# Kernel optimization log

Hardware: AMD Instinct MI355X
Metric: run time of the kernel (lower is better)

## Reference

```python
import jax, jax.numpy as jnp
import numpy as np

B, T, D, H_, N_ = 4, 1024, 2048, 32, 64


def setup_inputs() -> dict:
    key = jax.random.key(0)
    keys = iter(jax.random.split(key, 40))

    def rn(shape, s):
        return (jax.random.normal(next(keys), shape, jnp.float32) * s)

    inp = {
        'x': rn((B, T, D), 1.0),
        'x_prev': jnp.zeros((B, D), jnp.float32),
        'v_first': rn((B, T, D), 1.0),
        'state': jnp.zeros((B, H_, N_, N_), jnp.float32),
        'x_r': rn((1, 1, D), 0.1), 'x_w': rn((1, 1, D), 0.1), 'x_k': rn((1, 1, D), 0.1),
        'x_v': rn((1, 1, D), 0.1), 'x_a': rn((1, 1, D), 0.1), 'x_g': rn((1, 1, D), 0.1),
        'w0': rn((1, 1, D), 0.5),
        'w1': rn((D, 64), 0.02), 'w2': rn((64, D), 0.02),
        'a0': rn((1, 1, D), 0.5),
        'a1': rn((D, 64), 0.02), 'a2': rn((64, D), 0.02),
        'v0': rn((1, 1, D), 0.5),
        'v1': rn((D, 32), 0.02), 'v2': rn((32, D), 0.02),
        'g1': rn((D, 128), 0.02), 'g2': rn((128, D), 0.02),
        'k_k': rn((1, 1, D), 0.5), 'k_a': rn((1, 1, D), 0.5),
        'r_k': rn((D,), 0.5),
        'R_': rn((D, D), 0.02), 'K_': rn((D, D), 0.02),
        'V_': rn((D, D), 0.02), 'O_': rn((D, D), 0.02),
        'ln_w': jnp.ones((D,), jnp.float32),
        'ln_b': jnp.zeros((D,), jnp.float32),
        'H': H_, 'N': N_, 'layer_id': 1,
    }
    return inp


def reference(x, x_prev, v_first, state, x_r, x_w, x_k, x_v, x_a, x_g,
              w0, w1, w2, a0, a1, a2, v0, v1, v2, g1, g2,
              k_k, k_a, r_k, R_, K_, V_, O_, ln_w, ln_b, H, N, layer_id):
    B, T, D = x.shape
    # token shift
    xx = jnp.concatenate([x_prev[:, None, :], x[:, :-1]], axis=1) - x
    xr = x + xx * x_r; xw = x + xx * x_w; xk = x + xx * x_k
    xv = x + xx * x_v; xa = x + xx * x_a; xg = x + xx * x_g

    r = xr @ R_
    # decay: exp(-e^{-0.5} * sigmoid(.)) == exp(-exp(logsigmoid(.) - 0.5))
    w = jnp.exp(-0.606531 * jax.nn.sigmoid(w0 + jnp.tanh(xw @ w1) @ w2))
    k = xk @ K_
    v = xv @ V_
    a = jax.nn.sigmoid(a0 + (xa @ a1) @ a2)
    g = jax.nn.sigmoid(xg @ g1) @ g2

    kk4 = (k * k_k).reshape(B, T, H, N)
    kk4 = kk4 / jnp.maximum(jnp.linalg.norm(kk4, axis=-1, keepdims=True), 1e-12)
    kk = kk4.reshape(B, T, D)
    k = k * (1 + (a - 1) * k_a)
    if layer_id == 0:
        v_first = v
    else:
        v = v + (v_first - v) * jax.nn.sigmoid(v0 + (xv @ v1) @ v2)

    aa = -kk
    bb = kk * a

    def to_tbhn(t):
        return t.reshape(B, T, H, N).transpose(1, 0, 2, 3)

    rs, ws, ks, vs, aas, bbs = map(to_tbhn, (r, w, k, v, aa, bb))

    def step(st, inp):
        r_t, w_t, k_t, v_t, a_t, b_t = inp
        ab = jnp.einsum('bhi,bhj->bhij', a_t, b_t)      # rank-1 removal/add
        vk = jnp.einsum('bhi,bhj->bhij', v_t, k_t)
        st = st * w_t[:, :, None, :] + jnp.einsum('bhik,bhkj->bhij', st, ab) + vk
        y = jnp.einsum('bhij,bhj->bhi', st, r_t)        # state @ r
        return st, y

    state_f, ys = jax.lax.scan(step, state, (rs, ws, ks, vs, aas, bbs))
    y = ys.transpose(1, 0, 2, 3)  # [B,T,H,N]

    # torch group_norm on [B, H*N, T]: normalize each (b,h) group over (N,T)
    mean = y.mean(axis=(1, 3), keepdims=True)
    var = y.var(axis=(1, 3), keepdims=True)
    y = (y - mean) / jnp.sqrt(var + 0.00064)
    y = y * ln_w.reshape(1, 1, H, N) + ln_b.reshape(1, 1, H, N)

    bonus = (r * k * r_k).reshape(B, T, H, N).sum(-1, keepdims=True) * v.reshape(B, T, H, N)
    xx_fin = (y + bonus).reshape(B, T, D)
    out = (xx_fin * g) @ O_
    return out, x[:, -1], state_f, v_first
```

## Files before the change

kernel.cpp:

```cpp
#include <hip/hip_runtime.h>
#include <math.h>
#include <stdint.h>

#define B_ 4
#define T_ 1024
#define D_ 2048
#define H_ 32
#define N_ 64
static constexpr size_t BTD = (size_t)B_ * T_ * D_;

typedef __attribute__((ext_vector_type(8))) short short8;
typedef __attribute__((ext_vector_type(4))) float floatx4;

typedef __attribute__((address_space(3))) unsigned int       lds_u32;
typedef __attribute__((address_space(1))) const unsigned int glb_u32;

__device__ __forceinline__ void async_cp16(const unsigned short* g, unsigned short* l) {
  __builtin_amdgcn_global_load_lds((glb_u32*)g, (lds_u32*)l, 16, 0, 0);
}

__device__ __forceinline__ unsigned short f2bf(float f) {
  union { float f; unsigned int u; } v; v.f = f;
  unsigned int r = v.u + 0x7fffu + ((v.u >> 16) & 1u);
  return (unsigned short)(r >> 16);
}

__device__ __forceinline__ float bf2f(unsigned short u) {
  union { unsigned int u; float f; } v; v.u = (unsigned int)u << 16;
  return v.f;
}

__device__ __forceinline__ void store_bf4(unsigned short* dst, float a, float b, float c, float d) {
  unsigned long long v = (unsigned long long)f2bf(a) | ((unsigned long long)f2bf(b) << 16)
                       | ((unsigned long long)f2bf(c) << 32) | ((unsigned long long)f2bf(d) << 48);
  *(unsigned long long*)dst = v;
}

__device__ __forceinline__ void ld_bf8(const unsigned short* p, float* o) {
  union { short8 v; unsigned short u[8]; } t;
  t.v = *(const short8*)p;
#pragma unroll
  for (int c = 0; c < 8; ++c) o[c] = bf2f(t.u[c]);
}

__device__ __forceinline__ void cv4(uint2 r, float* o) {
  union { unsigned int u; float f; } t;
  t.u = r.x << 16;         o[0] = t.f;
  t.u = r.x & 0xffff0000u; o[1] = t.f;
  t.u = r.y << 16;         o[2] = t.f;
  t.u = r.y & 0xffff0000u; o[3] = t.f;
}

__device__ __forceinline__ float sigm(float z) { return 1.f / (1.f + expf(-z)); }

__global__ __launch_bounds__(256)
void mix_kernel(const float* __restrict__ x, const float* __restrict__ xprev,
                const float* __restrict__ coef, unsigned short* __restrict__ out)
{
  size_t i4 = (size_t)blockIdx.x * 256 + threadIdx.x;
  size_t e = i4 * 4;
  if (e >= BTD) return;
  int d = (int)(e & (D_ - 1));
  size_t bt = e >> 11;
  int t = (int)(bt & (T_ - 1));
  float4 xv = *(const float4*)(x + e);
  float4 xs;
  if (t == 0) xs = *(const float4*)(xprev + ((bt >> 10) << 11) + d);
  else        xs = *(const float4*)(x + e - D_);
  float4 cf = *(const float4*)(coef + d);
  float o0 = xv.x + (xs.x - xv.x) * cf.x;
  float o1 = xv.y + (xs.y - xv.y) * cf.y;
  float o2 = xv.z + (xs.z - xv.z) * cf.z;
  float o3 = xv.w + (xs.w - xv.w) * cf.w;
  store_bf4(out + e, o0, o1, o2, o3);
}

__global__ __launch_bounds__(256)
void transpose_bf16(const float* sA, const float* sB, const float* sC, const float* sD,
                    unsigned short* dA, unsigned short* dB, unsigned short* dC, unsigned short* dD,
                    int R, int C, int Cout)
{
  const float* src = blockIdx.z == 0 ? sA : blockIdx.z == 1 ? sB : blockIdx.z == 2 ? sC : sD;
  unsigned short* dst = blockIdx.z == 0 ? dA : blockIdx.z == 1 ? dB : blockIdx.z == 2 ? dC : dD;
  __shared__ float tile[64][65];
  int rBase = blockIdx.x * 64;
  int cBase = blockIdx.y * 64;
  int tid = threadIdx.x;
  int tc = tid & 63, tr4 = tid >> 6;
#pragma unroll
  for (int jj = 0; jj < 16; ++jj) {
    int r = rBase + jj * 4 + tr4;
    int c = cBase + tc;
    float v = (r < R && c < C) ? src[(size_t)r * C + c] : 0.f;
    tile[jj * 4 + tr4][tc] = v;
  }
  __syncthreads();
#pragma unroll
  for (int jj = 0; jj < 16; ++jj) {
    int cl = jj * 4 + tr4;
    int rl = tc;
    int c = cBase + cl, r = rBase + rl;
    if (c < Cout && r < R)
      dst[(size_t)c * R + r] = f2bf(tile[rl][cl]);
  }
}

template<int EPI>
__global__ __launch_bounds__(256, 2)
void gemm_bt(const unsigned short* __restrict__ A, const unsigned short* __restrict__ BT,
             float* __restrict__ Cf, unsigned short* __restrict__ Cb,
             int K, int ldc, int Nout, const float* __restrict__ bias)
{
  __shared__ unsigned short lA[128 * 32];
  __shared__ unsigned short lB[128 * 32];
  int tid = threadIdx.x;
  int lane = tid & 63;
  int wv = tid >> 6;
  int wrow = wv >> 1, wcol = wv & 1;
  int mBase = blockIdx.x * 128;
  int nBase = blockIdx.y * 128;
  int r16 = lane & 15, q = lane >> 4;

  floatx4 acc[4][4];
  floatx4 zero = {0.f, 0.f, 0.f, 0.f};
#pragma unroll
  for (int i = 0; i < 4; i++)
#pragma unroll
    for (int j = 0; j < 4; j++) acc[i][j] = zero;

  int arow = tid >> 2, ach = (tid & 3) * 8;
  const unsigned short* ga0 = A  + (size_t)(mBase + arow) * K + ach;
  const unsigned short* ga1 = A  + (size_t)(mBase + 64 + arow) * K + ach;
  const unsigned short* gb0 = BT + (size_t)(nBase + arow) * K + ach;
  const unsigned short* gb1 = BT + (size_t)(nBase + 64 + arow) * K + ach;
  unsigned short* la0 = lA + tid * 8;
  unsigned short* la1 = lA + 2048 + tid * 8;
  unsigned short* lb0 = lB + tid * 8;
  unsigned short* lb1 = lB + 2048 + tid * 8;

  for (int kb = 0; kb < K; kb += 32) {
    async_cp16(ga0 + kb, la0);
    async_cp16(ga1 + kb, la1);
    async_cp16(gb0 + kb, lb0);
    async_cp16(gb1 + kb, lb1);
    __syncthreads();
    short8 af[4], bf[4];
#pragma unroll
    for (int i = 0; i < 4; i++)
      af[i] = *(const short8*)(lA + (wrow * 64 + i * 16 + r16) * 32 + q * 8);
#pragma unroll
    for (int j = 0; j < 4; j++)
      bf[j] = *(const short8*)(lB + (wcol * 64 + j * 16 + r16) * 32 + q * 8);
#pragma unroll
    for (int i = 0; i < 4; i++)
#pragma unroll
      for (int j = 0; j < 4; j++)
        acc[i][j] = __builtin_amdgcn_mfma_f32_16x16x32_bf16(af[i], bf[j], acc[i][j], 0, 0, 0);
    __syncthreads();
  }

#pragma unroll
  for (int i = 0; i < 4; i++) {
    int r0 = mBase + wrow * 64 + i * 16 + q * 4;
#pragma unroll
    for (int j = 0; j < 4; j++) {
      int c = nBase + wcol * 64 + j * 16 + r16;
#pragma unroll
      for (int rg = 0; rg < 4; rg++) {
        float v = acc[i][j][rg];
        size_t idx = (size_t)(r0 + rg) * ldc + c;
        if (EPI == 0) {
          Cf[idx] = v;
        } else if (EPI == 1) {
          if (c < Nout) Cb[idx] = f2bf(tanhf(v));
        } else if (EPI == 2) {
          if (c < Nout) Cb[idx] = f2bf(sigm(v));
        } else if (EPI == 3) {
          if (c < Nout) Cb[idx] = f2bf(v);
        } else if (EPI == 6) {
          Cb[idx] = f2bf(sigm(bias[c] + v));
        } else if (EPI == 7) {
          Cb[idx] = f2bf(expf(-0.606531f * sigm(bias[c] + v)));
        }
      }
    }
  }
}

__global__ __launch_bounds__(256)
void prep_kernel(unsigned short* __restrict__ kb, unsigned short* __restrict__ ab,
                 float* __restrict__ vb, unsigned short* __restrict__ vmb,
                 const float* __restrict__ vfirst, const float* __restrict__ kkc,
                 const float* __restrict__ kac, const int* __restrict__ layer)
{
  int g = blockIdx.x * 4 + (threadIdx.x >> 6);
  int n = threadIdx.x & 63;
  size_t idx = (size_t)g * 64 + n;
  int d = ((g & (H_ - 1)) << 6) + n;
  float kr = bf2f(kb[idx]);
  float av = bf2f(ab[idx]);
  float vr = vb[idx];
  float vm = bf2f(vmb[idx]);
  float vf = vfirst[idx];
  float kkv = kr * kkc[d];
  float ss = kkv * kkv;
#pragma unroll
  for (int m = 1; m < 64; m <<= 1) ss += __shfl_xor(ss, m);
  float nrm = fmaxf(sqrtf(ss), 1e-12f);
  kkv = kkv / nrm;
  float kf = kr * (1.f + (av - 1.f) * kac[d]);
  float vfin = (*layer == 0) ? vr : vr + (vf - vr) * vm;
  kb[idx] = f2bf(kf);
  vb[idx] = vfin;
  ab[idx] = f2bf(-kkv);
  vmb[idx] = f2bf(kkv * av);
}

__global__ __launch_bounds__(256, 2)
void scan_kernel(const unsigned short* __restrict__ rb, const unsigned short* __restrict__ wb,
                 const unsigned short* __restrict__ kb, const float* __restrict__ vb,
                 const unsigned short* __restrict__ ab, const unsigned short* __restrict__ bbv,
                 const float* __restrict__ s0, float* __restrict__ yb,
                 float* __restrict__ sf)
{
  int blk = blockIdx.x;
  int bh = blk >> 2;
  int quarter = blk & 3;
  int b = bh >> 5, h = bh & 31;
  int tid = threadIdx.x;
  int lane = tid & 63;
  int wvi = tid >> 6;
  int i = quarter * 16 + wvi * 4 + (lane >> 4);
  int p = lane & 15;
  int co = p * 4;

  float st[4];
  {
    const float* sp = s0 + ((size_t)bh * 64 + i) * 64 + co;
    *(float4*)st = *(const float4*)sp;
  }
  size_t base = (size_t)b * T_ * D_ + h * 64;
  const unsigned short* pr = rb + base + co;
  const unsigned short* pw = wb + base + co;
  const unsigned short* pk = kb + base + co;
  const unsigned short* pa = ab + base + co;
  const unsigned short* pb = bbv + base + co;
  const float* pv = vb + base + i;
  float* py = yb + base + i;

  uint2 rgR[8], rgW[8], rgK[8], rgA[8], rgB[8];
  float rgV[8];
#pragma unroll
  for (int s = 0; s < 8; ++s) {
    size_t o = (size_t)s * D_;
    rgR[s] = *(const uint2*)(pr + o);
    rgW[s] = *(const uint2*)(pw + o);
    rgK[s] = *(const uint2*)(pk + o);
    rgA[s] = *(const uint2*)(pa + o);
    rgB[s] = *(const uint2*)(pb + o);
    rgV[s] = pv[o];
  }

  for (int tb = 0; tb < T_; tb += 8) {
#pragma unroll
    for (int s = 0; s < 8; ++s) {
      int t = tb + s;
      size_t o = (size_t)t * D_;
      float av[4], wv4[4], kv[4], bv[4], rv[4];
      cv4(rgA[s], av);
      cv4(rgW[s], wv4);
      cv4(rgK[s], kv);
      cv4(rgB[s], bv);
      cv4(rgR[s], rv);
      float vi = rgV[s];

      int tn = t + 8;
      size_t on = (size_t)(tn < T_ ? tn : 0) * D_;
      rgR[s] = *(const uint2*)(pr + on);
      rgW[s] = *(const uint2*)(pw + on);
      rgK[s] = *(const uint2*)(pk + on);
      rgA[s] = *(const uint2*)(pa + on);
      rgB[s] = *(const uint2*)(pb + on);
      rgV[s] = pv[on];

      float sa = 0.f;
#pragma unroll
      for (int c = 0; c < 4; ++c) sa = fmaf(st[c], av[c], sa);
      sa += __shfl_xor(sa, 1);
      sa += __shfl_xor(sa, 2);
      sa += __shfl_xor(sa, 4);
      sa += __shfl_xor(sa, 8);

#pragma unroll
      for (int c = 0; c < 4; ++c)
        st[c] = fmaf(st[c], wv4[c], fmaf(vi, kv[c], sa * bv[c]));

      float y = 0.f;
#pragma unroll
      for (int c = 0; c < 4; ++c) y = fmaf(st[c], rv[c], y);
      y += __shfl_xor(y, 1);
      y += __shfl_xor(y, 2);
      y += __shfl_xor(y, 4);
      y += __shfl_xor(y, 8);
      if (p == 0) py[o] = y;
    }
  }

  float* sp = sf + ((size_t)bh * 64 + i) * 64 + co;
  *(float4*)sp = *(float4*)st;
}

__global__ __launch_bounds__(256)
void gn_stats(const float* __restrict__ yb, float* __restrict__ gn)
{
  int bh = blockIdx.x;
  int b = bh >> 5, h = bh & 31;
  int tid = threadIdx.x;
  int lane = tid & 63, wv = tid >> 6;
  size_t base = (size_t)b * T_ * D_ + h * 64;
  int n = tid & 63, t0 = tid >> 6;
  float s = 0.f, s2 = 0.f;
  for (int t = t0; t < T_; t += 4) {
    float v = yb[base + (size_t)t * D_ + n];
    s += v; s2 += v * v;
  }
#pragma unroll
  for (int m = 1; m < 64; m <<= 1) { s += __shfl_xor(s, m); s2 += __shfl_xor(s2, m); }
  __shared__ float ls[4], ls2[4];
  if (lane == 0) { ls[wv] = s; ls2[wv] = s2; }
  __syncthreads();
  if (tid == 0) {
    float S = ls[0] + ls[1] + ls[2] + ls[3];
    float S2 = ls2[0] + ls2[1] + ls2[2] + ls2[3];
    float mean = S * (1.f / 65536.f);
    float var = S2 * (1.f / 65536.f) - mean * mean;
    gn[2 * bh] = mean;
    gn[2 * bh + 1] = rsqrtf(var + 0.00064f);
  }
}

__global__ __launch_bounds__(256)
void final_mix(const float* __restrict__ yb, const float* __restrict__ gn,
               const unsigned short* __restrict__ rb, const unsigned short* __restrict__ kb,
               const float* __restrict__ vb, const unsigned short* __restrict__ gb,
               const float* __restrict__ lnw, const float* __restrict__ lnb,
               const float* __restrict__ rk, unsigned short* __restrict__ af)
{
  int bt = blockIdx.x;
  int b = bt >> 10;
  size_t base = (size_t)bt * D_;
  int tid = threadIdx.x;
  int d0 = tid * 8;

  float rr[8], kv[8], qv[8];
  ld_bf8(rb + base + d0, rr);
  ld_bf8(kb + base + d0, kv);
  *(float4*)&qv[0] = *(const float4*)(rk + d0);
  *(float4*)&qv[4] = *(const float4*)(rk + d0 + 4);
  float part = 0.f;
#pragma unroll
  for (int c = 0; c < 8; ++c) part = fmaf(rr[c] * kv[c], qv[c], part);
  part += __shfl_xor(part, 1);
  part += __shfl_xor(part, 2);
  part += __shfl_xor(part, 4);
  __shared__ float red[32];
  if ((tid & 7) == 0) red[tid >> 3] = part;
  __syncthreads();
  int h = tid >> 3;
  float bs = red[h];
  float mean = gn[2 * (b * H_ + h)], istd = gn[2 * (b * H_ + h) + 1];

  float yv[8], vv[8], gg[8], lw[8], lb2[8];
  *(float4*)&yv[0] = *(const float4*)(yb + base + d0);
  *(float4*)&yv[4] = *(const float4*)(yb + base + d0 + 4);
  *(float4*)&vv[0] = *(const float4*)(vb + base + d0);
  *(float4*)&vv[4] = *(const float4*)(vb + base + d0 + 4);
  ld_bf8(gb + base + d0, gg);
  *(float4*)&lw[0] = *(const float4*)(lnw + d0);
  *(float4*)&lw[4] = *(const float4*)(lnw + d0 + 4);
  *(float4*)&lb2[0] = *(const float4*)(lnb + d0);
  *(float4*)&lb2[4] = *(const float4*)(lnb + d0 + 4);

  float o[8];
#pragma unroll
  for (int c = 0; c < 8; ++c)
    o[c] = (fmaf(yv[c] - mean, istd * lw[c], lb2[c]) + bs * vv[c]) * gg[c];
  store_bf4(af + base + d0, o[0], o[1], o[2], o[3]);
  store_bf4(af + base + d0 + 4, o[4], o[5], o[6], o[7]);
}

__global__ __launch_bounds__(256)
void tail_copy(const float* __restrict__ x, const float* __restrict__ vf_in,
               const float* __restrict__ vfin, const int* __restrict__ layer,
               float* __restrict__ oxl, float* __restrict__ ovf)
{
  size_t i4 = (size_t)blockIdx.x * 256 + threadIdx.x;
  size_t e = i4 * 4;
  if (e >= BTD) return;
  int lay = *layer;
  float4 s = (lay == 0) ? *(const float4*)(vfin + e) : *(const float4*)(vf_in + e);
  *(float4*)(ovf + e) = s;
  if (e < (size_t)B_ * D_) {
    size_t b = e >> 11;
    size_t d = e & (D_ - 1);
    *(float4*)(oxl + e) = *(const float4*)(x + (b * T_ + T_ - 1) * (size_t)D_ + d);
  }
}

extern "C" void kernel_launch(void* const* d_in, const int* in_sizes, int n_in,
                              void* d_out, int out_size, void* d_ws, size_t ws_size,
                              hipStream_t stream)
{
  const float* x       = (const float*)d_in[0];
  const float* x_prev  = (const float*)d_in[1];
  const float* v_first = (const float*)d_in[2];
  const float* state0  = (const float*)d_in[3];
  const float* x_r = (const float*)d_in[4];
  const float* x_w = (const float*)d_in[5];
  const float* x_k = (const float*)d_in[6];
  const float* x_v = (const float*)d_in[7];
  const float* x_a = (const float*)d_in[8];
  const float* x_g = (const float*)d_in[9];
  const float* w0 = (const float*)d_in[10];
  const float* w1 = (const float*)d_in[11];
  const float* w2 = (const float*)d_in[12];
  const float* a0 = (const float*)d_in[13];
  const float* a1 = (const float*)d_in[14];
  const float* a2 = (const float*)d_in[15];
  const float* v0 = (const float*)d_in[16];
  const float* v1 = (const float*)d_in[17];
  const float* v2 = (const float*)d_in[18];
  const float* g1 = (const float*)d_in[19];
  const float* g2 = (const float*)d_in[20];
  const float* k_k = (const float*)d_in[21];
  const float* k_a = (const float*)d_in[22];
  const float* r_k = (const float*)d_in[23];
  const float* Rm = (const float*)d_in[24];
  const float* Km = (const float*)d_in[25];
  const float* Vm = (const float*)d_in[26];
  const float* Om = (const float*)d_in[27];
  const float* ln_w = (const float*)d_in[28];
  const float* ln_b = (const float*)d_in[29];
  const int* layer = (const int*)d_in[32];

  float* out        = (float*)d_out;
  float* out_xlast  = out + BTD;
  float* out_state  = out_xlast + (size_t)B_ * D_;
  float* out_vfirst = out_state + (size_t)B_ * H_ * N_ * N_;

  float* ybuf = out;
  float* vbuf = out_vfirst;

  char* p = (char*)d_ws;
  auto alloc = [&](size_t bytes) { void* r = p; p += (bytes + 255) & ~(size_t)255; return r; };

  unsigned short* r_bf = (unsigned short*)alloc(BTD * 2);
  unsigned short* k_bf = (unsigned short*)alloc(BTD * 2);
  unsigned short* w_bf = (unsigned short*)alloc(BTD * 2);
  unsigned short* a_bf = (unsigned short*)alloc(BTD * 2);
  unsigned short* m_bf = (unsigned short*)alloc(BTD * 2);
  unsigned short* g_bf = (unsigned short*)alloc(BTD * 2);
  unsigned short* xm   = (unsigned short*)alloc(BTD * 2);
  unsigned short* btR  = (unsigned short*)alloc((size_t)D_ * D_ * 2);
  unsigned short* btK  = (unsigned short*)alloc((size_t)D_ * D_ * 2);
  unsigned short* btV  = (unsigned short*)alloc((size_t)D_ * D_ * 2);
  unsigned short* btO  = (unsigned short*)alloc((size_t)D_ * D_ * 2);
  unsigned short* btw1 = (unsigned short*)alloc((size_t)128 * D_ * 2);
  unsigned short* bta1 = (unsigned short*)alloc((size_t)128 * D_ * 2);
  unsigned short* btv1 = (unsigned short*)alloc((size_t)128 * D_ * 2);
  unsigned short* btg1 = (unsigned short*)alloc((size_t)128 * D_ * 2);
  unsigned short* btw2 = (unsigned short*)alloc((size_t)D_ * 64 * 2);
  unsigned short* bta2 = (unsigned short*)alloc((size_t)D_ * 64 * 2);
  unsigned short* btv2 = (unsigned short*)alloc((size_t)D_ * 32 * 2);
  unsigned short* btg2 = (unsigned short*)alloc((size_t)D_ * 128 * 2);
  unsigned short* h1w  = (unsigned short*)alloc((size_t)B_ * T_ * 64 * 2);
  unsigned short* h1a  = (unsigned short*)alloc((size_t)B_ * T_ * 64 * 2);
  unsigned short* h1v  = (unsigned short*)alloc((size_t)B_ * T_ * 32 * 2);
  unsigned short* h1g  = (unsigned short*)alloc((size_t)B_ * T_ * 128 * 2);
  float* gnbuf = (float*)alloc(256 * 4);
  (void)ws_size; (void)in_sizes; (void)n_in; (void)out_size;

  const int MIXG = (int)(BTD / 4 / 256);

  transpose_bf16<<<dim3(32, 32, 4), 256, 0, stream>>>(Rm, Km, Vm, Om, btR, btK, btV, btO, D_, D_, D_);
  transpose_bf16<<<dim3(32, 2, 2), 256, 0, stream>>>(w1, a1, nullptr, nullptr, btw1, bta1, nullptr, nullptr, D_, 64, 128);
  transpose_bf16<<<dim3(32, 2, 1), 256, 0, stream>>>(v1, nullptr, nullptr, nullptr, btv1, nullptr, nullptr, nullptr, D_, 32, 128);
  transpose_bf16<<<dim3(32, 2, 1), 256, 0, stream>>>(g1, nullptr, nullptr, nullptr, btg1, nullptr, nullptr, nullptr, D_, 128, 128);
  transpose_bf16<<<dim3(1, 32, 2), 256, 0, stream>>>(w2, a2, nullptr, nullptr, btw2, bta2, nullptr, nullptr, 64, D_, D_);
  transpose_bf16<<<dim3(1, 32, 1), 256, 0, stream>>>(v2, nullptr, nullptr, nullptr, btv2, nullptr, nullptr, nullptr, 32, D_, D_);
  transpose_bf16<<<dim3(2, 32, 1), 256, 0, stream>>>(g2, nullptr, nullptr, nullptr, btg2, nullptr, nullptr, nullptr, 128, D_, D_);

  mix_kernel<<<MIXG, 256, 0, stream>>>(x, x_prev, x_r, xm);
  gemm_bt<3><<<dim3(32, 16), 256, 0, stream>>>(xm, btR, nullptr, r_bf, D_, D_, D_, nullptr);
  mix_kernel<<<MIXG, 256, 0, stream>>>(x, x_prev, x_k, xm);
  gemm_bt<3><<<dim3(32, 16), 256, 0, stream>>>(xm, btK, nullptr, k_bf, D_, D_, D_, nullptr);
  mix_kernel<<<MIXG, 256, 0, stream>>>(x, x_prev, x_v, xm);
  gemm_bt<0><<<dim3(32, 16), 256, 0, stream>>>(xm, btV, vbuf, nullptr, D_, D_, D_, nullptr);
  gemm_bt<3><<<dim3(32, 1), 256, 0, stream>>>(xm, btv1, nullptr, h1v, D_, 32, 32, nullptr);
  mix_kernel<<<MIXG, 256, 0, stream>>>(x, x_prev, x_w, xm);
  gemm_bt<1><<<dim3(32, 1), 256, 0, stream>>>(xm, btw1, nullptr, h1w, D_, 64, 64, nullptr);
  mix_kernel<<<MIXG, 256, 0, stream>>>(x, x_prev, x_a, xm);
  gemm_bt<3><<<dim3(32, 1), 256, 0, stream>>>(xm, bta1, nullptr, h1a, D_, 64, 64, nullptr);
  mix_kernel<<<MIXG, 256, 0, stream>>>(x, x_prev, x_g, xm);
  gemm_bt<2><<<dim3(32, 1), 256, 0, stream>>>(xm, btg1, nullptr, h1g, D_, 128, 128, nullptr);

  gemm_bt<7><<<dim3(32, 16), 256, 0, stream>>>(h1w, btw2, nullptr, w_bf, 64, D_, D_, w0);
  gemm_bt<6><<<dim3(32, 16), 256, 0, stream>>>(h1a, bta2, nullptr, a_bf, 64, D_, D_, a0);
  gemm_bt<6><<<dim3(32, 16), 256, 0, stream>>>(h1v, btv2, nullptr, m_bf, 32, D_, D_, v0);
  gemm_bt<3><<<dim3(32, 16), 256, 0, stream>>>(h1g, btg2, nullptr, g_bf, 128, D_, D_, nullptr);

  prep_kernel<<<32768, 256, 0, stream>>>(k_bf, a_bf, vbuf, m_bf, v_first, k_k, k_a, layer);

  scan_kernel<<<512, 256, 0, stream>>>(r_bf, w_bf, k_bf, vbuf, a_bf, m_bf, state0, ybuf, out_state);

  gn_stats<<<128, 256, 0, stream>>>(ybuf, gnbuf);
  final_mix<<<B_ * T_, 256, 0, stream>>>(ybuf, gnbuf, r_bf, k_bf, vbuf, g_bf, ln_w, ln_b, r_k, xm);
  gemm_bt<0><<<dim3(32, 16), 256, 0, stream>>>(xm, btO, out, nullptr, D_, D_, D_, nullptr);

  tail_copy<<<MIXG, 256, 0, stream>>>(x, v_first, vbuf, layer, out_xlast, out_vfirst);
}
```

Measured before the change: 1.359 ms.

## Batch projection GEMMs via grid z, fuse token-mix kernels, split scan finer

Replaces six per-coefficient mix launches with two mix3 kernels that each compute three token-shift mixes from one x read. The R/K/V GEMMs, the three LoRA-down GEMMs and the four LoRA-up GEMMs are each batched into a single launch indexed by blockIdx.z, which fills the GPU better and cuts launch count. LoRA buffers are padded to 128 columns, with zeros written into the padding. The scan kernel now gives each thread 2 state columns instead of 4 across 1024 blocks with occupancy hint 4, raising parallelism on the serial recurrence at the cost of one extra shuffle stage per reduction. Buffers are reused (w_bf/a_bf alias mix buffers), which relies on launch ordering for correctness.

```diff
diff --git a/kernel.cpp b/kernel.cpp
--- a/kernel.cpp
+++ b/kernel.cpp
@@ -43,22 +43,22 @@
   for (int c = 0; c < 8; ++c) o[c] = bf2f(t.u[c]);
 }
 
-__device__ __forceinline__ void cv4(uint2 r, float* o) {
+__device__ __forceinline__ void cv2(unsigned int r, float* o) {
   union { unsigned int u; float f; } t;
-  t.u = r.x << 16;         o[0] = t.f;
-  t.u = r.x & 0xffff0000u; o[1] = t.f;
-  t.u = r.y << 16;         o[2] = t.f;
-  t.u = r.y & 0xffff0000u; o[3] = t.f;
+  t.u = r << 16;         o[0] = t.f;
+  t.u = r & 0xffff0000u; o[1] = t.f;
 }
 
 __device__ __forceinline__ float sigm(float z) { return 1.f / (1.f + expf(-z)); }
 
 __global__ __launch_bounds__(256)
-void mix_kernel(const float* __restrict__ x, const float* __restrict__ xprev,
-                const float* __restrict__ coef, unsigned short* __restrict__ out)
-{
-  size_t i4 = (size_t)blockIdx.x * 256 + threadIdx.x;
-  size_t e = i4 * 4;
+void mix3_kernel(const float* __restrict__ x, const float* __restrict__ xprev,
+                 const float* __restrict__ c0, const float* __restrict__ c1,
+                 const float* __restrict__ c2,
+                 unsigned short* __restrict__ o0, unsigned short* __restrict__ o1,
+                 unsigned short* __restrict__ o2)
+{
+  size_t e = ((size_t)blockIdx.x * 256 + threadIdx.x) * 4;
   if (e >= BTD) return;
   int d = (int)(e & (D_ - 1));
   size_t bt = e >> 11;
@@ -67,18 +67,21 @@
   float4 xs;
   if (t == 0) xs = *(const float4*)(xprev + ((bt >> 10) << 11) + d);
   else        xs = *(const float4*)(x + e - D_);
-  float4 cf = *(const float4*)(coef + d);
-  float o0 = xv.x + (xs.x - xv.x) * cf.x;
-  float o1 = xv.y + (xs.y - xv.y) * cf.y;
-  float o2 = xv.z + (xs.z - xv.z) * cf.z;
-  float o3 = xv.w + (xs.w - xv.w) * cf.w;
-  store_bf4(out + e, o0, o1, o2, o3);
+  float dx0 = xs.x - xv.x, dx1 = xs.y - xv.y, dx2 = xs.z - xv.z, dx3 = xs.w - xv.w;
+
+  float4 cf;
+  cf = *(const float4*)(c0 + d);
+  store_bf4(o0 + e, xv.x + dx0 * cf.x, xv.y + dx1 * cf.y, xv.z + dx2 * cf.z, xv.w + dx3 * cf.w);
+  cf = *(const float4*)(c1 + d);
+  store_bf4(o1 + e, xv.x + dx0 * cf.x, xv.y + dx1 * cf.y, xv.z + dx2 * cf.z, xv.w + dx3 * cf.w);
+  cf = *(const float4*)(c2 + d);
+  store_bf4(o2 + e, xv.x + dx0 * cf.x, xv.y + dx1 * cf.y, xv.z + dx2 * cf.z, xv.w + dx3 * cf.w);
 }
 
 __global__ __launch_bounds__(256)
 void transpose_bf16(const float* sA, const float* sB, const float* sC, const float* sD,
                     unsigned short* dA, unsigned short* dB, unsigned short* dC, unsigned short* dD,
-                    int R, int C, int Cout)
+                    int R, int C, int Cout, int Rout)
 {
   const float* src = blockIdx.z == 0 ? sA : blockIdx.z == 1 ? sB : blockIdx.z == 2 ? sC : sD;
   unsigned short* dst = blockIdx.z == 0 ? dA : blockIdx.z == 1 ? dB : blockIdx.z == 2 ? dC : dD;
@@ -100,19 +103,16 @@
     int cl = jj * 4 + tr4;
     int rl = tc;
     int c = cBase + cl, r = rBase + rl;
-    if (c < Cout && r < R)
-      dst[(size_t)c * R + r] = f2bf(tile[rl][cl]);
-  }
-}
-
-template<int EPI>
-__global__ __launch_bounds__(256, 2)
-void gemm_bt(const unsigned short* __restrict__ A, const unsigned short* __restrict__ BT,
-             float* __restrict__ Cf, unsigned short* __restrict__ Cb,
-             int K, int ldc, int Nout, const float* __restrict__ bias)
-{
-  __shared__ unsigned short lA[128 * 32];
-  __shared__ unsigned short lB[128 * 32];
+    if (c < Cout && r < Rout)
+      dst[(size_t)c * Rout + r] = f2bf(tile[rl][cl]);
+  }
+}
+
+__device__ __forceinline__ void gemm_core(const unsigned short* __restrict__ A,
+                                          const unsigned short* __restrict__ BT,
+                                          int K, unsigned short* lA, unsigned short* lB,
+                                          floatx4 (&acc)[4][4])
+{
   int tid = threadIdx.x;
   int lane = tid & 63;
   int wv = tid >> 6;
@@ -121,7 +121,6 @@
   int nBase = blockIdx.y * 128;
   int r16 = lane & 15, q = lane >> 4;
 
-  floatx4 acc[4][4];
   floatx4 zero = {0.f, 0.f, 0.f, 0.f};
 #pragma unroll
   for (int i = 0; i < 4; i++)
@@ -158,7 +157,29 @@
         acc[i][j] = __builtin_amdgcn_mfma_f32_16x16x32_bf16(af[i], bf[j], acc[i][j], 0, 0, 0);
     __syncthreads();
   }
-
+}
+
+#define GEMM_EPILOGUE_HEAD                                        \
+  int tid = threadIdx.x;                                          \
+  int lane = tid & 63;                                            \
+  int wv = tid >> 6;                                              \
+  int wrow = wv >> 1, wcol = wv & 1;                              \
+  int mBase = blockIdx.x * 128;                                   \
+  int nBase = blockIdx.y * 128;                                   \
+  int r16 = lane & 15, q = lane >> 4;                             \
+  (void)lane;
+
+template<int EPI>
+__global__ __launch_bounds__(256, 2)
+void gemm_bt(const unsigned short* __restrict__ A, const unsigned short* __restrict__ BT,
+             float* __restrict__ Cf, unsigned short* __restrict__ Cb,
+             int K, int ldc, int Nout)
+{
+  __shared__ unsigned short lA[128 * 32];
+  __shared__ unsigned short lB[128 * 32];
+  floatx4 acc[4][4];
+  gemm_core(A, BT, K, lA, lB, acc);
+  GEMM_EPILOGUE_HEAD
 #pragma unroll
   for (int i = 0; i < 4; i++) {
     int r0 = mBase + wrow * 64 + i * 16 + q * 4;
@@ -169,19 +190,116 @@
       for (int rg = 0; rg < 4; rg++) {
         float v = acc[i][j][rg];
         size_t idx = (size_t)(r0 + rg) * ldc + c;
-        if (EPI == 0) {
-          Cf[idx] = v;
-        } else if (EPI == 1) {
-          if (c < Nout) Cb[idx] = f2bf(tanhf(v));
-        } else if (EPI == 2) {
-          if (c < Nout) Cb[idx] = f2bf(sigm(v));
-        } else if (EPI == 3) {
-          if (c < Nout) Cb[idx] = f2bf(v);
-        } else if (EPI == 6) {
-          Cb[idx] = f2bf(sigm(bias[c] + v));
-        } else if (EPI == 7) {
-          Cb[idx] = f2bf(expf(-0.606531f * sigm(bias[c] + v)));
-        }
+        if (EPI == 0) Cf[idx] = v;
+        else          Cb[idx] = f2bf(c < Nout ? v : 0.f);
+      }
+    }
+  }
+}
+
+__global__ __launch_bounds__(256, 2)
+void gemm_rkv(const unsigned short* __restrict__ xr, const unsigned short* __restrict__ xk,
+              const unsigned short* __restrict__ xv,
+              const unsigned short* __restrict__ btR, const unsigned short* __restrict__ btK,
+              const unsigned short* __restrict__ btV,
+              unsigned short* __restrict__ r_bf, unsigned short* __restrict__ k_bf,
+              float* __restrict__ vbuf)
+{
+  __shared__ unsigned short lA[128 * 32];
+  __shared__ unsigned short lB[128 * 32];
+  int z = blockIdx.z;
+  const unsigned short* A  = z == 0 ? xr  : z == 1 ? xk  : xv;
+  const unsigned short* BT = z == 0 ? btR : z == 1 ? btK : btV;
+  floatx4 acc[4][4];
+  gemm_core(A, BT, D_, lA, lB, acc);
+  GEMM_EPILOGUE_HEAD
+  unsigned short* db = z == 0 ? r_bf : k_bf;
+#pragma unroll
+  for (int i = 0; i < 4; i++) {
+    int r0 = mBase + wrow * 64 + i * 16 + q * 4;
+#pragma unroll
+    for (int j = 0; j < 4; j++) {
+      int c = nBase + wcol * 64 + j * 16 + r16;
+#pragma unroll
+      for (int rg = 0; rg < 4; rg++) {
+        float v = acc[i][j][rg];
+        size_t idx = (size_t)(r0 + rg) * D_ + c;
+        if (z == 2) vbuf[idx] = v;
+        else        db[idx] = f2bf(v);
+      }
+    }
+  }
+}
+
+__global__ __launch_bounds__(256, 2)
+void gemm_lora1(const unsigned short* __restrict__ xw, const unsigned short* __restrict__ xa,
+                const unsigned short* __restrict__ xg,
+                const unsigned short* __restrict__ btw1, const unsigned short* __restrict__ bta1,
+                const unsigned short* __restrict__ btg1,
+                unsigned short* __restrict__ h1w, unsigned short* __restrict__ h1a,
+                unsigned short* __restrict__ h1g)
+{
+  __shared__ unsigned short lA[128 * 32];
+  __shared__ unsigned short lB[128 * 32];
+  int z = blockIdx.z;
+  const unsigned short* A  = z == 0 ? xw   : z == 1 ? xa   : xg;
+  const unsigned short* BT = z == 0 ? btw1 : z == 1 ? bta1 : btg1;
+  unsigned short* dst      = z == 0 ? h1w  : z == 1 ? h1a  : h1g;
+  int Nout = z == 2 ? 128 : 64;
+  floatx4 acc[4][4];
+  gemm_core(A, BT, D_, lA, lB, acc);
+  GEMM_EPILOGUE_HEAD
+#pragma unroll
+  for (int i = 0; i < 4; i++) {
+    int r0 = mBase + wrow * 64 + i * 16 + q * 4;
+#pragma unroll
+    for (int j = 0; j < 4; j++) {
+      int c = nBase + wcol * 64 + j * 16 + r16;
+#pragma unroll
+      for (int rg = 0; rg < 4; rg++) {
+        float v = acc[i][j][rg];
+        if (z == 0) v = tanhf(v);
+        else if (z == 2) v = sigm(v);
+        size_t idx = (size_t)(r0 + rg) * 128 + c;
+        dst[idx] = f2bf(c < Nout ? v : 0.f);
+      }
+    }
+  }
+}
+
+__global__ __launch_bounds__(256, 2)
+void gemm_lora2(const unsigned short* __restrict__ h1w, const unsigned short* __restrict__ h1a,
+                const unsigned short* __restrict__ h1v, const unsigned short* __restrict__ h1g,
+                const unsigned short* __restrict__ btw2, const unsigned short* __restrict__ bta2,
+                const unsigned short* __restrict__ btv2, const unsigned short* __restrict__ btg2,
+                unsigned short* __restrict__ w_bf, unsigned short* __restrict__ a_bf,
+                unsigned short* __restrict__ m_bf, unsigned short* __restrict__ g_bf,
+                const float* __restrict__ w0, const float* __restrict__ a0,
+                const float* __restrict__ v0)
+{
+  __shared__ unsigned short lA[128 * 32];
+  __shared__ unsigned short lB[128 * 32];
+  int z = blockIdx.z;
+  const unsigned short* A  = z == 0 ? h1w  : z == 1 ? h1a  : z == 2 ? h1v  : h1g;
+  const unsigned short* BT = z == 0 ? btw2 : z == 1 ? bta2 : z == 2 ? btv2 : btg2;
+  unsigned short* dst      = z == 0 ? w_bf : z == 1 ? a_bf : z == 2 ? m_bf : g_bf;
+  const float* bias        = z == 0 ? w0   : z == 1 ? a0   : z == 2 ? v0   : nullptr;
+  floatx4 acc[4][4];
+  gemm_core(A, BT, 128, lA, lB, acc);
+  GEMM_EPILOGUE_HEAD
+#pragma unroll
+  for (int i = 0; i < 4; i++) {
+    int r0 = mBase + wrow * 64 + i * 16 + q * 4;
+#pragma unroll
+    for (int j = 0; j < 4; j++) {
+      int c = nBase + wcol * 64 + j * 16 + r16;
+#pragma unroll
+      for (int rg = 0; rg < 4; rg++) {
+        float v = acc[i][j][rg];
+        if (z == 0)      v = expf(-0.606531f * sigm(bias[c] + v));
+        else if (z < 3)  v = sigm(bias[c] + v);
+        size_t idx = (size_t)(r0 + rg) * D_ + c;
+        dst[idx] = f2bf(v);
       }
     }
   }
@@ -216,7 +334,7 @@
   vmb[idx] = f2bf(kkv * av);
 }
 
-__global__ __launch_bounds__(256, 2)
+__global__ __launch_bounds__(256, 4)
 void scan_kernel(const unsigned short* __restrict__ rb, const unsigned short* __restrict__ wb,
                  const unsigned short* __restrict__ kb, const float* __restrict__ vb,
                  const unsigned short* __restrict__ ab, const unsigned short* __restrict__ bbv,
@@ -224,20 +342,21 @@
                  float* __restrict__ sf)
 {
   int blk = blockIdx.x;
-  int bh = blk >> 2;
-  int quarter = blk & 3;
+  int bh = blk >> 3;
+  int oct = blk & 7;
   int b = bh >> 5, h = bh & 31;
   int tid = threadIdx.x;
   int lane = tid & 63;
   int wvi = tid >> 6;
-  int i = quarter * 16 + wvi * 4 + (lane >> 4);
-  int p = lane & 15;
-  int co = p * 4;
-
-  float st[4];
+  int i = oct * 8 + wvi * 2 + (lane >> 5);
+  int p = lane & 31;
+  int co = p * 2;
+
+  float st[2];
   {
     const float* sp = s0 + ((size_t)bh * 64 + i) * 64 + co;
-    *(float4*)st = *(const float4*)sp;
+    float2 s2 = *(const float2*)sp;
+    st[0] = s2.x; st[1] = s2.y;
   }
   size_t base = (size_t)b * T_ * D_ + h * 64;
   const unsigned short* pr = rb + base + co;
@@ -248,16 +367,16 @@
   const float* pv = vb + base + i;
   float* py = yb + base + i;
 
-  uint2 rgR[8], rgW[8], rgK[8], rgA[8], rgB[8];
+  unsigned int rgR[8], rgW[8], rgK[8], rgA[8], rgB[8];
   float rgV[8];
 #pragma unroll
   for (int s = 0; s < 8; ++s) {
     size_t o = (size_t)s * D_;
-    rgR[s] = *(const uint2*)(pr + o);
-    rgW[s] = *(const uint2*)(pw + o);
-    rgK[s] = *(const uint2*)(pk + o);
-    rgA[s] = *(const uint2*)(pa + o);
-    rgB[s] = *(const uint2*)(pb + o);
+    rgR[s] = *(const unsigned int*)(pr + o);
+    rgW[s] = *(const unsigned int*)(pw + o);
+    rgK[s] = *(const unsigned int*)(pk + o);
+    rgA[s] = *(const unsigned int*)(pa + o);
+    rgB[s] = *(const unsigned int*)(pb + o);
     rgV[s] = pv[o];
   }
 
@@ -266,48 +385,45 @@
     for (int s = 0; s < 8; ++s) {
       int t = tb + s;
       size_t o = (size_t)t * D_;
-      float av[4], wv4[4], kv[4], bv[4], rv[4];
-      cv4(rgA[s], av);
-      cv4(rgW[s], wv4);
-      cv4(rgK[s], kv);
-      cv4(rgB[s], bv);
-      cv4(rgR[s], rv);
+      float av[2], wv2[2], kv[2], bv[2], rv[2];
+      cv2(rgA[s], av);
+      cv2(rgW[s], wv2);
+      cv2(rgK[s], kv);
+      cv2(rgB[s], bv);
+      cv2(rgR[s], rv);
       float vi = rgV[s];
 
       int tn = t + 8;
       size_t on = (size_t)(tn < T_ ? tn : 0) * D_;
-      rgR[s] = *(const uint2*)(pr + on);
-      rgW[s] = *(const uint2*)(pw + on);
-      rgK[s] = *(const uint2*)(pk + on);
-      rgA[s] = *(const uint2*)(pa + on);
-      rgB[s] = *(const uint2*)(pb + on);
+      rgR[s] = *(const unsigned int*)(pr + on);
+      rgW[s] = *(const unsigned int*)(pw + on);
+      rgK[s] = *(const unsigned int*)(pk + on);
+      rgA[s] = *(const unsigned int*)(pa + on);
+      rgB[s] = *(const unsigned int*)(pb + on);
       rgV[s] = pv[on];
 
-      float sa = 0.f;
-#pragma unroll
-      for (int c = 0; c < 4; ++c) sa = fmaf(st[c], av[c], sa);
+      float sa = fmaf(st[0], av[0], st[1] * av[1]);
       sa += __shfl_xor(sa, 1);
       sa += __shfl_xor(sa, 2);
       sa += __shfl_xor(sa, 4);
       sa += __shfl_xor(sa, 8);
-
-#pragma unroll
-      for (int c = 0; c < 4; ++c)
-        st[c] = fmaf(st[c], wv4[c], fmaf(vi, kv[c], sa * bv[c]));
-
-      float y = 0.f;
-#pragma unroll
-      for (int c = 0; c < 4; ++c) y = fmaf(st[c], rv[c], y);
+      sa += __shfl_xor(sa, 16);
+
+      st[0] = fmaf(st[0], wv2[0], fmaf(vi, kv[0], sa * bv[0]));
+      st[1] = fmaf(st[1], wv2[1], fmaf(vi, kv[1], sa * bv[1]));
+
+      float y = fmaf(st[0], rv[0], st[1] * rv[1]);
       y += __shfl_xor(y, 1);
       y += __shfl_xor(y, 2);
       y += __shfl_xor(y, 4);
       y += __shfl_xor(y, 8);
+      y += __shfl_xor(y, 16);
       if (p == 0) py[o] = y;
     }
   }
 
   float* sp = sf + ((size_t)bh * 64 + i) * 64 + co;
-  *(float4*)sp = *(float4*)st;
+  *(float2*)sp = make_float2(st[0], st[1]);
 }
 
 __global__ __launch_bounds__(256)
@@ -394,8 +510,7 @@
                const float* __restrict__ vfin, const int* __restrict__ layer,
                float* __restrict__ oxl, float* __restrict__ ovf)
 {
-  size_t i4 = (size_t)blockIdx.x * 256 + threadIdx.x;
-  size_t e = i4 * 4;
+  size_t e = ((size_t)blockIdx.x * 256 + threadIdx.x) * 4;
   if (e >= BTD) return;
   int lay = *layer;
   float4 s = (lay == 0) ? *(const float4*)(vfin + e) : *(const float4*)(vf_in + e);
@@ -454,13 +569,15 @@
   char* p = (char*)d_ws;
   auto alloc = [&](size_t bytes) { void* r = p; p += (bytes + 255) & ~(size_t)255; return r; };
 
+  unsigned short* mix0 = (unsigned short*)alloc(BTD * 2);
+  unsigned short* mix1 = (unsigned short*)alloc(BTD * 2);
+  unsigned short* mix2 = (unsigned short*)alloc(BTD * 2);
   unsigned short* r_bf = (unsigned short*)alloc(BTD * 2);
   unsigned short* k_bf = (unsigned short*)alloc(BTD * 2);
-  unsigned short* w_bf = (unsigned short*)alloc(BTD * 2);
-  unsigned short* a_bf = (unsigned short*)alloc(BTD * 2);
   unsigned short* m_bf = (unsigned short*)alloc(BTD * 2);
   unsigned short* g_bf = (unsigned short*)alloc(BTD * 2);
-  unsigned short* xm   = (unsigned short*)alloc(BTD * 2);
+  unsigned short* w_bf = mix1;
+  unsigned short* a_bf = mix2;
   unsigned short* btR  = (unsigned short*)alloc((size_t)D_ * D_ * 2);
   unsigned short* btK  = (unsigned short*)alloc((size_t)D_ * D_ * 2);
   unsigned short* btV  = (unsigned short*)alloc((size_t)D_ * D_ * 2);
@@ -469,53 +586,43 @@
   unsigned short* bta1 = (unsigned short*)alloc((size_t)128 * D_ * 2);
   unsigned short* btv1 = (unsigned short*)alloc((size_t)128 * D_ * 2);
   unsigned short* btg1 = (unsigned short*)alloc((size_t)128 * D_ * 2);
-  unsigned short* btw2 = (unsigned short*)alloc((size_t)D_ * 64 * 2);
-  unsigned short* bta2 = (unsigned short*)alloc((size_t)D_ * 64 * 2);
-  unsigned short* btv2 = (unsigned short*)alloc((size_t)D_ * 32 * 2);
+  unsigned short* btw2 = (unsigned short*)alloc((size_t)D_ * 128 * 2);
+  unsigned short* bta2 = (unsigned short*)alloc((size_t)D_ * 128 * 2);
+  unsigned short* btv2 = (unsigned short*)alloc((size_t)D_ * 128 * 2);
   unsigned short* btg2 = (unsigned short*)alloc((size_t)D_ * 128 * 2);
-  unsigned short* h1w  = (unsigned short*)alloc((size_t)B_ * T_ * 64 * 2);
-  unsigned short* h1a  = (unsigned short*)alloc((size_t)B_ * T_ * 64 * 2);
-  unsigned short* h1v  = (unsigned short*)alloc((size_t)B_ * T_ * 32 * 2);
+  unsigned short* h1w  = (unsigned short*)alloc((size_t)B_ * T_ * 128 * 2);
+  unsigned short* h1a  = (unsigned short*)alloc((size_t)B_ * T_ * 128 * 2);
+  unsigned short* h1v  = (unsigned short*)alloc((size_t)B_ * T_ * 128 * 2);
   unsigned short* h1g  = (unsigned short*)alloc((size_t)B_ * T_ * 128 * 2);
   float* gnbuf = (float*)alloc(256 * 4);
   (void)ws_size; (void)in_sizes; (void)n_in; (void)out_size;
 
   const int MIXG = (int)(BTD / 4 / 256);
 
-  transpose_bf16<<<dim3(32, 32, 4), 256, 0, stream>>>(Rm, Km, Vm, Om, btR, btK, btV, btO, D_, D_, D_);
-  transpose_bf16<<<dim3(32, 2, 2), 256, 0, stream>>>(w1, a1, nullptr, nullptr, btw1, bta1, nullptr, nullptr, D_, 64, 128);
-  transpose_bf16<<<dim3(32, 2, 1), 256, 0, stream>>>(v1, nullptr, nullptr, nullptr, btv1, nullptr, nullptr, nullptr, D_, 32, 128);
-  transpose_bf16<<<dim3(32, 2, 1), 256, 0, stream>>>(g1, nullptr, nullptr, nullptr, btg1, nullptr, nullptr, nullptr, D_, 128, 128);
-  transpose_bf16<<<dim3(1, 32, 2), 256, 0, stream>>>(w2, a2, nullptr, nullptr, btw2, bta2, nullptr, nullptr, 64, D_, D_);
-  transpose_bf16<<<dim3(1, 32, 1), 256, 0, stream>>>(v2, nullptr, nullptr, nullptr, btv2, nullptr, nullptr, nullptr, 32, D_, D_);
-  transpose_bf16<<<dim3(2, 32, 1), 256, 0, stream>>>(g2, nullptr, nullptr, nullptr, btg2, nullptr, nullptr, nullptr, 128, D_, D_);
-
-  mix_kernel<<<MIXG, 256, 0, stream>>>(x, x_prev, x_r, xm);
-  gemm_bt<3><<<dim3(32, 16), 256, 0, stream>>>(xm, btR, nullptr, r_bf, D_, D_, D_, nullptr);
-  mix_kernel<<<MIXG, 256, 0, stream>>>(x, x_prev, x_k, xm);
-  gemm_bt<3><<<dim3(32, 16), 256, 0, stream>>>(xm, btK, nullptr, k_bf, D_, D_, D_, nullptr);
-  mix_kernel<<<MIXG, 256, 0, stream>>>(x, x_prev, x_v, xm);
-  gemm_bt<0><<<dim3(32, 16), 256, 0, stream>>>(xm, btV, vbuf, nullptr, D_, D_, D_, nullptr);
-  gemm_bt<3><<<dim3(32, 1), 256, 0, stream>>>(xm, btv1, nullptr, h1v, D_, 32, 32, nullptr);
-  mix_kernel<<<MIXG, 256, 0, stream>>>(x, x_prev, x_w, xm);
-  gemm_bt<1><<<dim3(32, 1), 256, 0, stream>>>(xm, btw1, nullptr, h1w, D_, 64, 64, nullptr);
-  mix_kernel<<<MIXG, 256, 0, stream>>>(x, x_prev, x_a, xm);
-  gemm_bt<3><<<dim3(32, 1), 256, 0, stream>>>(xm, bta1, nullptr, h1a, D_, 64, 64, nullptr);
-  mix_kernel<<<MIXG, 256, 0, stream>>>(x, x_prev, x_g, xm);
-  gemm_bt<2><<<dim3(32, 1), 256, 0, stream>>>(xm, btg1, nullptr, h1g, D_, 128, 128, nullptr);
-
-  gemm_bt<7><<<dim3(32, 16), 256, 0, stream>>>(h1w, btw2, nullptr, w_bf, 64, D_, D_, w0);
-  gemm_bt<6><<<dim3(32, 16), 256, 0, stream>>>(h1a, bta2, nullptr, a_bf, 64, D_, D_, a0);
-  gemm_bt<6><<<dim3(32, 16), 256, 0, stream>>>(h1v, btv2, nullptr, m_bf, 32, D_, D_, v0);
-  gemm_bt<3><<<dim3(32, 16), 256, 0, stream>>>(h1g, btg2, nullptr, g_bf, 128, D_, D_, nullptr);
+  transpose_bf16<<<dim3(32, 32, 4), 256, 0, stream>>>(Rm, Km, Vm, Om, btR, btK, btV, btO, D_, D_, D_, D_);
+  transpose_bf16<<<dim3(32, 2, 2), 256, 0, stream>>>(w1, a1, nullptr, nullptr, btw1, bta1, nullptr, nullptr, D_, 64, 128, D_);
+  transpose_bf16<<<dim3(32, 2, 1), 256, 0, stream>>>(v1, nullptr, nullptr, nullptr, btv1, nullptr, nullptr, nullptr, D_, 32, 128, D_);
+  transpose_bf16<<<dim3(32, 2, 1), 256, 0, stream>>>(g1, nullptr, nullptr, nullptr, btg1, nullptr, nullptr, nullptr, D_, 128, 128, D_);
+  transpose_bf16<<<dim3(2, 32, 2), 256, 0, stream>>>(w2, a2, nullptr, nullptr, btw2, bta2, nullptr, nullptr, 64, D_, D_, 128);
+  transpose_bf16<<<dim3(2, 32, 1), 256, 0, stream>>>(v2, nullptr, nullptr, nullptr, btv2, nullptr, nullptr, nullptr, 32, D_, D_, 128);
+  transpose_bf16<<<dim3(2, 32, 1), 256, 0, stream>>>(g2, nullptr, nullptr, nullptr, btg2, nullptr, nullptr, nullptr, 128, D_, D_, 128);
+
+  mix3_kernel<<<MIXG, 256, 0, stream>>>(x, x_prev, x_r, x_k, x_v, mix0, mix1, mix2);
+  gemm_rkv<<<dim3(32, 16, 3), 256, 0, stream>>>(mix0, mix1, mix2, btR, btK, btV, r_bf, k_bf, vbuf);
+  gemm_bt<3><<<dim3(32, 1), 256, 0, stream>>>(mix2, btv1, nullptr, h1v, D_, 128, 32);
+
+  mix3_kernel<<<MIXG, 256, 0, stream>>>(x, x_prev, x_w, x_a, x_g, mix0, mix1, mix2);
+  gemm_lora1<<<dim3(32, 1, 3), 256, 0, stream>>>(mix0, mix1, mix2, btw1, bta1, btg1, h1w, h1a, h1g);
+  gemm_lora2<<<dim3(32, 16, 4), 256, 0, stream>>>(h1w, h1a, h1v, h1g, btw2, bta2, btv2, btg2,
+                                                  w_bf, a_bf, m_bf, g_bf, w0, a0, v0);
 
   prep_kernel<<<32768, 256, 0, stream>>>(k_bf, a_bf, vbuf, m_bf, v_first, k_k, k_a, layer);
 
-  scan_kernel<<<512, 256, 0, stream>>>(r_bf, w_bf, k_bf, vbuf, a_bf, m_bf, state0, ybuf, out_state);
+  scan_kernel<<<1024, 256, 0, stream>>>(r_bf, w_bf, k_bf, vbuf, a_bf, m_bf, state0, ybuf, out_state);
 
   gn_stats<<<128, 256, 0, stream>>>(ybuf, gnbuf);
-  final_mix<<<B_ * T_, 256, 0, stream>>>(ybuf, gnbuf, r_bf, k_bf, vbuf, g_bf, ln_w, ln_b, r_k, xm);
-  gemm_bt<0><<<dim3(32, 16), 256, 0, stream>>>(xm, btO, out, nullptr, D_, D_, D_, nullptr);
+  final_mix<<<B_ * T_, 256, 0, stream>>>(ybuf, gnbuf, r_bf, k_bf, vbuf, g_bf, ln_w, ln_b, r_k, mix0);
+  gemm_bt<0><<<dim3(32, 16), 256, 0, stream>>>(mix0, btO, out, nullptr, D_, D_, D_);
 
   tail_copy<<<MIXG, 256, 0, stream>>>(x, v_first, vbuf, layer, out_xlast, out_vfirst);
 }
```

Result: faster. 1.269 ms (-6.6%).
